# Kernel optimization log

Measured on AMD Instinct MI355X. Metric: run time of the kernel, lower is better.

The kernel has to match this reference:

```python
import jax, jax.numpy as jnp
import numpy as np

B, L, M = 256, 8, 1024  # batch, input_length (= window), latent dim m
P = 8                   # predict_length


def setup_inputs() -> dict:
    key = jax.random.key(0)
    k1, k2, k3 = jax.random.split(key, 3)
    x = jax.random.normal(k1, (B, L, M), dtype=jnp.float32)
    # A initialized near identity (original init is torch.eye repeated), plus
    # small noise so the test is non-trivial and the recurrence stays stable.
    eye = jnp.broadcast_to(jnp.eye(M, dtype=jnp.float32), (L, M, M))
    A_real = eye / L + 0.02 * jax.random.normal(k2, (L, M, M), dtype=jnp.float32)
    A_imag = 0.02 * jax.random.normal(k3, (L, M, M), dtype=jnp.float32)
    return {"x": x, "A_real": A_real, "A_imag": A_imag, "predict_length": P}


def reference(x, A_real, A_imag, predict_length):
    # Complex DMD operator bank: A[j] is [M, M] cfloat.
    A = (A_real + 1j * A_imag).astype(jnp.complex64)
    Lw = x.shape[1]
    # Original inner loop: u2 += A[j] @ uc[:, -j]  (note -0 == 0!)
    #   j=0 pairs A[0] with window position 0; j>=1 pairs A[j] with position Lw-j.
    # Re-index so term for window position p uses Ag[p]: Ag[0]=A[0], Ag[p]=A[Lw-p].
    idx = jnp.concatenate([jnp.array([0]), jnp.arange(Lw - 1, 0, -1)])
    Ag = A[idx]  # [Lw, M, M]

    uc0 = x.astype(jnp.complex64)  # [B, Lw, M] sliding window state

    def step(uc, _):
        # Fused accumulation: sum_p Ag[p] @ uc[:, p]  -> [B, M]
        u2 = jnp.einsum("kmn,bkn->bm", Ag, uc)
        uc = jnp.concatenate([uc[:, 1:], u2[:, None]], axis=1)  # slide window
        return uc, None

    uc, _ = jax.lax.scan(step, uc0, None, length=predict_length)
    # Original casts cfloat -> double, which drops the imaginary part; keep fp32.
    return jnp.real(uc).astype(jnp.float32)
```

## Files before the change

### kernel.cpp

```cpp
#include <hip/hip_runtime.h>


#define LW 8

typedef __attribute__((ext_vector_type(8))) short  short8;
typedef __attribute__((ext_vector_type(8))) __bf16 bf16x8;
typedef __attribute__((ext_vector_type(4))) float  f32x4;
typedef __attribute__((ext_vector_type(4))) float  f4;
typedef const __attribute__((address_space(1))) void gvoid_t;
typedef __attribute__((address_space(3))) void lvoid_t;

static __device__ __forceinline__ short f2bf(float f) {
  unsigned u = __builtin_bit_cast(unsigned, f);
  u += 0x7FFFu + ((u >> 16) & 1u);
  return (short)(u >> 16);
}
static __device__ __forceinline__ float bf2f(short s) {
  unsigned u = ((unsigned)(unsigned short)s) << 16;
  return __builtin_bit_cast(float, u);
}
static __device__ __forceinline__ f32x4 mfma16(short8 a, short8 b, f32x4 c) {
  return __builtin_amdgcn_mfma_f32_16x16x32_bf16(
      __builtin_bit_cast(bf16x8, a), __builtin_bit_cast(bf16x8, b), c, 0, 0, 0);
}

__global__ __launch_bounds__(1024) void prep_all(const float* __restrict__ x,
                                                 const float* __restrict__ Ar,
                                                 const float* __restrict__ Ai,
                                                 short* __restrict__ Sr2,
                                                 short* __restrict__ Si2,
                                                 short* __restrict__ WTr,
                                                 short* __restrict__ WTi) {
  const int bid = blockIdx.x;
  if (bid < 1024) {
    const int tg = bid * 1024 + threadIdx.x;
    const int sq = tg & 3, col = (tg >> 2) & 63, kcg = (tg >> 8) & 31;
    const int colt = (tg >> 13) & 15, p = tg >> 17;
    const int qn = sq ^ ((col >> 1) & 3);
    const int m = (colt << 6) + col, n0 = (kcg << 5) + (qn << 3);
    const int qm = (LW - p) & 7;
    const size_t src = ((size_t)((qm << 10) + m) << 10) + n0;
    f4 r0 = *(const f4*)(Ar + src), r1 = *(const f4*)(Ar + src + 4);
    f4 i0 = *(const f4*)(Ai + src), i1 = *(const f4*)(Ai + src + 4);
    short8 vr, vi;
#pragma unroll
    for (int j = 0; j < 4; ++j) {
      vr[j] = f2bf(r0[j]); vr[j + 4] = f2bf(r1[j]);
      vi[j] = f2bf(i0[j]); vi[j + 4] = f2bf(i1[j]);
    }
    *(short8*)(WTr + ((size_t)tg << 3)) = vr;
    *(short8*)(WTi + ((size_t)tg << 3)) = vi;
  } else {
    const int tg = (bid - 1024) * 1024 + threadIdx.x;
    const int qn = tg & 3, kc = (tg >> 2) & 31, b = (tg >> 7) & 255, s = tg >> 15;
    const float* xp = x + ((size_t)(b * LW + s) << 10) + (kc << 5) + (qn << 3);
    f4 x0 = *(const f4*)xp, x1 = *(const f4*)(xp + 4);
    short8 v;
#pragma unroll
    for (int j = 0; j < 4; ++j) { v[j] = f2bf(x0[j]); v[j + 4] = f2bf(x1[j]); }
    const int sq = qn ^ ((b >> 1) & 3);
    const size_t dst = ((size_t)s << 18) + (kc << 13) + (b << 5) + (sq << 3);
    *(short8*)(Sr2 + dst) = v;
    short8 z = {0, 0, 0, 0, 0, 0, 0, 0};
    *(short8*)(Si2 + dst) = z;
  }
}


#define LOADA(set_, kc_) do {                                                    \
    const int kg_ = ((ks << 4) + (kc_)) << 13;                                   \
    _Pragma("unroll")                                                            \
    for (int rf_ = 0; rf_ < 4; ++rf_) {                                          \
      aR[set_][rf_] = *(const short8*)(SrB + kg_ + aoffG[rf_]);                  \
      aI[set_][rf_] = *(const short8*)(SiB + kg_ + aoffG[rf_]);                  \
    }                                                                            \
  } while (0)

#define COMP(set_, kc_) do {                                                     \
    short8 bR_[2], bI_[2];                                                       \
    _Pragma("unroll")                                                            \
    for (int cf_ = 0; cf_ < 2; ++cf_) {                                          \
      bR_[cf_] = *(const short8*)(ldsW + ((kc_) << 11) + boffL[cf_]);            \
      bI_[cf_] = *(const short8*)(ldsW + 32768 + ((kc_) << 11) + boffL[cf_]);    \
    }                                                                            \
    _Pragma("unroll")                                                            \
    for (int rf_ = 0; rf_ < 4; ++rf_) {                                          \
      const short8 nI_ = aI[set_][rf_] ^ SGN;                                    \
      _Pragma("unroll")                                                          \
      for (int cf_ = 0; cf_ < 2; ++cf_) {                                        \
        accR[rf_][cf_] = mfma16(aR[set_][rf_], bR_[cf_], accR[rf_][cf_]);        \
        accR[rf_][cf_] = mfma16(nI_,           bI_[cf_], accR[rf_][cf_]);        \
        accI[rf_][cf_] = mfma16(aR[set_][rf_], bI_[cf_], accI[rf_][cf_]);        \
        accI[rf_][cf_] = mfma16(aI[set_][rf_], bR_[cf_], accI[rf_][cf_]);        \
      }                                                                          \
    }                                                                            \
  } while (0)

__global__ __launch_bounds__(512, 2) void gemm_step(const short* __restrict__ Sr2,
                                                    const short* __restrict__ Si2,
                                                    const short* __restrict__ WTr,
                                                    const short* __restrict__ WTi,
                                                    short* __restrict__ Pp,
                                                    int t) {
  __shared__ short ldsW[65536];

  const int bid   = blockIdx.x;
  const int p     = bid & 7;
  const int inner = bid >> 3;
  const int colt  = inner & 15;
  const int ks    = inner >> 4;
  const int s     = (p + t) & 7;

  const int tid = threadIdx.x, lane = tid & 63, w = tid >> 6;
  const int rw = w >> 1, cw = w & 1;
  const int l15 = lane & 15, q = lane >> 4;

  {
    const short* baseR = WTr + (((size_t)((p << 4) + colt)) << 16) + ((size_t)ks << 15);
    const short* baseI = WTi + (((size_t)((p << 4) + colt)) << 16) + ((size_t)ks << 15);
#pragma unroll
    for (int j = 0; j < 16; ++j) {
      const int gid  = (j << 9) + tid;
      const int arr  = gid >> 12;
      const int rem  = gid & 4095;
      const short* src = (arr ? baseI : baseR) + (rem << 3);
      __builtin_amdgcn_global_load_lds((gvoid_t*)src,
          (lvoid_t*)&ldsW[(arr << 15) + (rem << 3)], 16, 0, 0);
    }
  }

  const short* SrB = Sr2 + ((size_t)s << 18);
  const short* SiB = Si2 + ((size_t)s << 18);
  int aoffG[4], boffL[2];
#pragma unroll
  for (int rf = 0; rf < 4; ++rf) {
    const int row = (rw << 6) + (rf << 4) + l15;
    aoffG[rf] = (row << 5) + ((q ^ ((row >> 1) & 3)) << 3);
  }
#pragma unroll
  for (int cf = 0; cf < 2; ++cf) {
    const int col = (cw << 5) + (cf << 4) + l15;
    boffL[cf] = (col << 5) + ((q ^ ((col >> 1) & 3)) << 3);
  }

  f32x4 accR[4][2], accI[4][2];
  const f32x4 z4 = {0.f, 0.f, 0.f, 0.f};
#pragma unroll
  for (int a = 0; a < 4; ++a)
#pragma unroll
    for (int c = 0; c < 2; ++c) { accR[a][c] = z4; accI[a][c] = z4; }

  const short8 SGN = {(short)0x8000, (short)0x8000, (short)0x8000, (short)0x8000,
                      (short)0x8000, (short)0x8000, (short)0x8000, (short)0x8000};

  short8 aR[2][4], aI[2][4];

  LOADA(0, 0);
  __syncthreads();

#pragma unroll
  for (int kc = 0; kc < 16; ++kc) {
    if (kc < 15) LOADA((kc + 1) & 1, kc + 1);
    COMP(kc & 1, kc);
  }

  short* op = Pp + ((size_t)((((p << 1) + ks) << 4) + colt) << 15) + (tid << 3);
#pragma unroll
  for (int rf = 0; rf < 4; ++rf)
#pragma unroll
    for (int cf = 0; cf < 2; ++cf) {
      short8 sv;
#pragma unroll
      for (int rg = 0; rg < 4; ++rg) {
        sv[rg]     = f2bf(accR[rf][cf][rg]);
        sv[rg + 4] = f2bf(accI[rf][cf][rg]);
      }
      *(short8*)(op + ((size_t)((rf << 1) + cf) << 12)) = sv;
    }
}

__global__ __launch_bounds__(256) void reduce_step(const short* __restrict__ Pp,
                                                   short* __restrict__ Sr2,
                                                   short* __restrict__ Si2,
                                                   float* __restrict__ out,
                                                   int t) {
  const int r = blockIdx.x * 256 + threadIdx.x;
  const int tidg = r & 511, o = (r >> 9) & 7, colt = r >> 12;

  float sum[8] = {0.f, 0.f, 0.f, 0.f, 0.f, 0.f, 0.f, 0.f};
#pragma unroll
  for (int sl = 0; sl < 16; ++sl) {
    const short8 v = *(const short8*)(
        Pp + ((size_t)(((sl << 4) + colt) << 3) + o << 12) + (tidg << 3));
#pragma unroll
    for (int jj = 0; jj < 8; ++jj) sum[jj] += bf2f(v[jj]);
  }

  const int rf = o >> 1, cf = o & 1;
  const int lane = tidg & 63, w = tidg >> 6;
  const int rw = w >> 1, cw = w & 1;
  const int l15 = lane & 15, q = lane >> 4;
  const int row0 = (rw << 6) + (rf << 4) + (q << 2);
  const int col  = (colt << 6) + (cw << 5) + (cf << 4) + l15;
  const int kc = col >> 5, qn = (col >> 3) & 3, j = col & 7;

#pragma unroll
  for (int rg = 0; rg < 4; ++rg) {
    const int row = row0 + rg;
    out[((size_t)((row << 3) + t) << 10) + col] = sum[rg];
    const int sq = qn ^ ((row >> 1) & 3);
    const size_t idx = ((size_t)t << 18) + (kc << 13) + (row << 5) + (sq << 3) + j;
    Sr2[idx] = f2bf(sum[rg]);
    Si2[idx] = f2bf(sum[rg + 4]);
  }
}

extern "C" void kernel_launch(void* const* d_in, const int* in_sizes, int n_in,
                              void* d_out, int out_size, void* d_ws, size_t ws_size,
                              hipStream_t stream) {
  const float* x  = (const float*)d_in[0];
  const float* Ar = (const float*)d_in[1];
  const float* Ai = (const float*)d_in[2];
  float* out = (float*)d_out;

  char* ws = (char*)d_ws;
  if (ws_size < (60u << 20)) return;
  short* Sr2 = (short*)(ws);
  short* Si2 = (short*)(ws + (4u  << 20));
  short* WTr = (short*)(ws + (8u  << 20));
  short* WTi = (short*)(ws + (24u << 20));
  short* Pp  = (short*)(ws + (40u << 20));

  prep_all<<<dim3(1280), dim3(1024), 0, stream>>>(x, Ar, Ai, Sr2, Si2, WTr, WTi);
  for (int t = 0; t < 8; ++t) {
    gemm_step<<<dim3(256), dim3(512), 0, stream>>>(Sr2, Si2, WTr, WTi, Pp, t);
    reduce_step<<<dim3(256), dim3(256), 0, stream>>>(Pp, Sr2, Si2, out, t);
  }
}
```

Baseline: 240.8 us.

## Narrow GEMM column tiles to 32 and double block count

```diff
diff --git a/kernel.cpp b/kernel.cpp
--- a/kernel.cpp
+++ b/kernel.cpp
@@ -29,15 +29,15 @@
                                                  const float* __restrict__ Ai,
                                                  short* __restrict__ Sr2,
                                                  short* __restrict__ Si2,
-                                                 short* __restrict__ WTr,
-                                                 short* __restrict__ WTi) {
+                                                 short* __restrict__ Wr5,
+                                                 short* __restrict__ Wi5) {
   const int bid = blockIdx.x;
   if (bid < 1024) {
     const int tg = bid * 1024 + threadIdx.x;
-    const int sq = tg & 3, col = (tg >> 2) & 63, kcg = (tg >> 8) & 31;
-    const int colt = (tg >> 13) & 15, p = tg >> 17;
+    const int sq = tg & 3, col = (tg >> 2) & 31, kcg = (tg >> 7) & 31;
+    const int colt = (tg >> 12) & 31, p = tg >> 17;
     const int qn = sq ^ ((col >> 1) & 3);
-    const int m = (colt << 6) + col, n0 = (kcg << 5) + (qn << 3);
+    const int m = (colt << 5) + col, n0 = (kcg << 5) + (qn << 3);
     const int qm = (LW - p) & 7;
     const size_t src = ((size_t)((qm << 10) + m) << 10) + n0;
     f4 r0 = *(const f4*)(Ar + src), r1 = *(const f4*)(Ar + src + 4);
@@ -48,8 +48,8 @@
       vr[j] = f2bf(r0[j]); vr[j + 4] = f2bf(r1[j]);
       vi[j] = f2bf(i0[j]); vi[j + 4] = f2bf(i1[j]);
     }
-    *(short8*)(WTr + ((size_t)tg << 3)) = vr;
-    *(short8*)(WTi + ((size_t)tg << 3)) = vi;
+    *(short8*)(Wr5 + ((size_t)tg << 3)) = vr;
+    *(short8*)(Wi5 + ((size_t)tg << 3)) = vi;
   } else {
     const int tg = (bid - 1024) * 1024 + threadIdx.x;
     const int qn = tg & 3, kc = (tg >> 2) & 31, b = (tg >> 7) & 255, s = tg >> 15;
@@ -80,9 +80,10 @@
     short8 bR_[2], bI_[2];                                                       \
     _Pragma("unroll")                                                            \
     for (int cf_ = 0; cf_ < 2; ++cf_) {                                          \
-      bR_[cf_] = *(const short8*)(ldsW + ((kc_) << 11) + boffL[cf_]);            \
-      bI_[cf_] = *(const short8*)(ldsW + 32768 + ((kc_) << 11) + boffL[cf_]);    \
+      bR_[cf_] = *(const short8*)(ldsW + ((kc_) << 10) + boffL[cf_]);            \
+      bI_[cf_] = *(const short8*)(ldsW + 16384 + ((kc_) << 10) + boffL[cf_]);    \
     }                                                                            \
+    __builtin_amdgcn_s_setprio(1);                                               \
     _Pragma("unroll")                                                            \
     for (int rf_ = 0; rf_ < 4; ++rf_) {                                          \
       const short8 nI_ = aI[set_][rf_] ^ SGN;                                    \
@@ -94,38 +95,38 @@
         accI[rf_][cf_] = mfma16(aI[set_][rf_], bR_[cf_], accI[rf_][cf_]);        \
       }                                                                          \
     }                                                                            \
+    __builtin_amdgcn_s_setprio(0);                                               \
   } while (0)
 
-__global__ __launch_bounds__(512, 2) void gemm_step(const short* __restrict__ Sr2,
+__global__ __launch_bounds__(256, 2) void gemm_step(const short* __restrict__ Sr2,
                                                     const short* __restrict__ Si2,
-                                                    const short* __restrict__ WTr,
-                                                    const short* __restrict__ WTi,
+                                                    const short* __restrict__ Wr5,
+                                                    const short* __restrict__ Wi5,
                                                     short* __restrict__ Pp,
                                                     int t) {
-  __shared__ short ldsW[65536];
+  __shared__ short ldsW[32768];
 
   const int bid   = blockIdx.x;
   const int p     = bid & 7;
   const int inner = bid >> 3;
-  const int colt  = inner & 15;
-  const int ks    = inner >> 4;
+  const int colt  = inner & 31;
+  const int ks    = inner >> 5;
   const int s     = (p + t) & 7;
 
   const int tid = threadIdx.x, lane = tid & 63, w = tid >> 6;
-  const int rw = w >> 1, cw = w & 1;
   const int l15 = lane & 15, q = lane >> 4;
 
   {
-    const short* baseR = WTr + (((size_t)((p << 4) + colt)) << 16) + ((size_t)ks << 15);
-    const short* baseI = WTi + (((size_t)((p << 4) + colt)) << 16) + ((size_t)ks << 15);
+    const short* baseR = Wr5 + (((size_t)((p << 5) + colt)) << 15) + ((size_t)ks << 14);
+    const short* baseI = Wi5 + (((size_t)((p << 5) + colt)) << 15) + ((size_t)ks << 14);
 #pragma unroll
     for (int j = 0; j < 16; ++j) {
-      const int gid  = (j << 9) + tid;
-      const int arr  = gid >> 12;
-      const int rem  = gid & 4095;
+      const int gid  = (j << 8) + tid;
+      const int arr  = gid >> 11;
+      const int rem  = gid & 2047;
       const short* src = (arr ? baseI : baseR) + (rem << 3);
       __builtin_amdgcn_global_load_lds((gvoid_t*)src,
-          (lvoid_t*)&ldsW[(arr << 15) + (rem << 3)], 16, 0, 0);
+          (lvoid_t*)&ldsW[(arr << 14) + (rem << 3)], 16, 0, 0);
     }
   }
 
@@ -134,12 +135,12 @@
   int aoffG[4], boffL[2];
 #pragma unroll
   for (int rf = 0; rf < 4; ++rf) {
-    const int row = (rw << 6) + (rf << 4) + l15;
+    const int row = (w << 6) + (rf << 4) + l15;
     aoffG[rf] = (row << 5) + ((q ^ ((row >> 1) & 3)) << 3);
   }
 #pragma unroll
   for (int cf = 0; cf < 2; ++cf) {
-    const int col = (cw << 5) + (cf << 4) + l15;
+    const int col = (cf << 4) + l15;
     boffL[cf] = (col << 5) + ((q ^ ((col >> 1) & 3)) << 3);
   }
 
@@ -164,7 +165,7 @@
     COMP(kc & 1, kc);
   }
 
-  short* op = Pp + ((size_t)((((p << 1) + ks) << 4) + colt) << 15) + (tid << 3);
+  short* op = Pp + ((size_t)(((((p << 1) + ks) << 5) + colt) << 3) << 11) + (tid << 3);
 #pragma unroll
   for (int rf = 0; rf < 4; ++rf)
 #pragma unroll
@@ -175,7 +176,7 @@
         sv[rg]     = f2bf(accR[rf][cf][rg]);
         sv[rg + 4] = f2bf(accI[rf][cf][rg]);
       }
-      *(short8*)(op + ((size_t)((rf << 1) + cf) << 12)) = sv;
+      *(short8*)(op + ((size_t)((rf << 1) + cf) << 11)) = sv;
     }
 }
 
@@ -185,23 +186,22 @@
                                                    float* __restrict__ out,
                                                    int t) {
   const int r = blockIdx.x * 256 + threadIdx.x;
-  const int tidg = r & 511, o = (r >> 9) & 7, colt = r >> 12;
+  const int tidg = r & 255, o = (r >> 8) & 7, colt = r >> 11;
 
   float sum[8] = {0.f, 0.f, 0.f, 0.f, 0.f, 0.f, 0.f, 0.f};
 #pragma unroll
   for (int sl = 0; sl < 16; ++sl) {
     const short8 v = *(const short8*)(
-        Pp + ((size_t)(((sl << 4) + colt) << 3) + o << 12) + (tidg << 3));
+        Pp + ((size_t)((((sl << 5) + colt) << 3) + o) << 11) + (tidg << 3));
 #pragma unroll
     for (int jj = 0; jj < 8; ++jj) sum[jj] += bf2f(v[jj]);
   }
 
   const int rf = o >> 1, cf = o & 1;
   const int lane = tidg & 63, w = tidg >> 6;
-  const int rw = w >> 1, cw = w & 1;
   const int l15 = lane & 15, q = lane >> 4;
-  const int row0 = (rw << 6) + (rf << 4) + (q << 2);
-  const int col  = (colt << 6) + (cw << 5) + (cf << 4) + l15;
+  const int row0 = (w << 6) + (rf << 4) + (q << 2);
+  const int col  = (colt << 5) + (cf << 4) + l15;
   const int kc = col >> 5, qn = (col >> 3) & 3, j = col & 7;
 
 #pragma unroll
@@ -227,13 +227,13 @@
   if (ws_size < (60u << 20)) return;
   short* Sr2 = (short*)(ws);
   short* Si2 = (short*)(ws + (4u  << 20));
-  short* WTr = (short*)(ws + (8u  << 20));
-  short* WTi = (short*)(ws + (24u << 20));
+  short* Wr5 = (short*)(ws + (8u  << 20));
+  short* Wi5 = (short*)(ws + (24u << 20));
   short* Pp  = (short*)(ws + (40u << 20));
 
-  prep_all<<<dim3(1280), dim3(1024), 0, stream>>>(x, Ar, Ai, Sr2, Si2, WTr, WTi);
+  prep_all<<<dim3(1280), dim3(1024), 0, stream>>>(x, Ar, Ai, Sr2, Si2, Wr5, Wi5);
   for (int t = 0; t < 8; ++t) {
-    gemm_step<<<dim3(256), dim3(512), 0, stream>>>(Sr2, Si2, WTr, WTi, Pp, t);
+    gemm_step<<<dim3(512), dim3(256), 0, stream>>>(Sr2, Si2, Wr5, Wi5, Pp, t);
     reduce_step<<<dim3(256), dim3(256), 0, stream>>>(Pp, Sr2, Si2, out, t);
   }
 }
```

Result: faster. 231.0 us (-4.1%).
